# Performance work log

Measured on AMD Instinct MI355X. Metric: run time of the kernel, lower is better.

The kernel has to match this reference:

```python
import jax, jax.numpy as jnp
import numpy as np

B, L, D, HD = 4, 4096, 2048, 128

def setup_inputs() -> dict:
    key = jax.random.key(0)
    ks = jax.random.split(key, 9)
    s = 0.02  # keep logits in a sane range
    return {
        "x": jax.random.normal(ks[0], (B, L, D), jnp.float32),
        "Wq": jax.random.normal(ks[1], (D, HD), jnp.float32) * s,
        "bq": jax.random.normal(ks[2], (HD,), jnp.float32) * s,
        "Wk": jax.random.normal(ks[3], (D, HD), jnp.float32) * s,
        "bk": jax.random.normal(ks[4], (HD,), jnp.float32) * s,
        "Wv": jax.random.normal(ks[5], (D, HD), jnp.float32) * s,
        "bv": jax.random.normal(ks[6], (HD,), jnp.float32) * s,
        "Wo": jax.random.normal(ks[7], (HD, D), jnp.float32) * s,
        "bo": jax.random.normal(ks[8], (D,), jnp.float32) * s,
    }

def reference(x, Wq, bq, Wk, bk, Wv, bv, Wo, bo):
    # x: (B, L, D)
    q = x @ Wq + bq                      # (B, L, HD)
    k = x @ Wk + bk
    v = x @ Wv + bv
    hd = q.shape[-1]
    scores = jnp.einsum('bqd,bkd->bqk', q, k) / jnp.sqrt(jnp.float32(hd))
    Lq = x.shape[1]
    causal = jnp.tril(jnp.ones((Lq, Lq), dtype=bool))  # (L, L)
    scores = jnp.where(causal, scores, -jnp.inf)
    weights = jax.nn.softmax(scores, axis=-1)          # (B, L, L)
    out = jnp.einsum('bqk,bkd->bqd', weights, v)       # (B, L, HD)
    return out @ Wo + bo                               # (B, L, D)
```

## Files before the change

kernel.cpp:

```cpp
#include <hip/hip_runtime.h>

#define B_  4
#define L_  4096
#define D_  2048
#define HD_ 128
#define M_  (B_*L_)

typedef __attribute__((ext_vector_type(8))) short short8;
typedef __attribute__((ext_vector_type(4))) float f32x4;
typedef __attribute__((ext_vector_type(16))) float f32x16;
typedef __attribute__((ext_vector_type(4))) unsigned short u16x4;
typedef __attribute__((ext_vector_type(4))) unsigned int u32x4;
typedef unsigned short u16;

#define GLL16(g, l) __builtin_amdgcn_global_load_lds( \
    (const __attribute__((address_space(1))) void*)(g), \
    (__attribute__((address_space(3))) void*)(l), 16, 0, 0)

__device__ __forceinline__ u16 f2bf(float f){
  union { float f; unsigned u; } v; v.f = f;
  unsigned r = v.u + 0x7FFFu + ((v.u >> 16) & 1u);
  return (u16)(r >> 16);
}

__device__ __forceinline__ unsigned cvtpk_bf16(float a, float b){
  unsigned r;
  asm volatile("v_cvt_pk_bf16_f32 %0, %1, %2" : "=v"(r) : "v"(a), "v"(b));
  return r;
}

__global__ __launch_bounds__(256) void prep_kernel(
    const float* __restrict__ Wq, const float* __restrict__ Wk,
    const float* __restrict__ Wv, const float* __restrict__ Wo,
    u16* __restrict__ Wf_qkv, u16* __restrict__ Wf_o)
{
  __shared__ float T[64][68];
  const int tid = threadIdx.x;
  int tb = blockIdx.x;
  int mat = tb >> 6, tt = tb & 63;
  const float* src; int Rw, Cw, rt, ct;
  if (mat < 3) {
    src = (mat==0) ? Wq : (mat==1) ? Wk : Wv;
    Rw = D_; Cw = HD_; rt = tt >> 1; ct = tt & 1;
  } else {
    src = Wo;
    Rw = HD_; Cw = D_; rt = tt >> 5; ct = tt & 31;
  }
  int r0 = rt*64, c0 = ct*64;
  #pragma unroll
  for (int i=0;i<4;i++){
    int fid = i*256 + tid;
    int row = fid >> 4, c4 = (fid & 15) * 4;
    float4 v = *reinterpret_cast<const float4*>(src + (size_t)(r0+row)*Cw + c0 + c4);
    *reinterpret_cast<float4*>(&T[row][c4]) = v;
  }
  __syncthreads();
  #pragma unroll
  for (int i=0;i<2;i++){
    int sid = i*256 + tid;
    int crow = sid >> 3, k8 = (sid & 7) * 8;
    short8 o;
    #pragma unroll
    for (int j=0;j<8;j++) o[j] = (short)f2bf(T[k8+j][crow]);
    int K = r0 + k8;
    if (mat < 3) {
      int C = mat*128 + c0 + crow;
      int t2 = K >> 6, ks = (K >> 5) & 1, lh = (K >> 3) & 3;
      int g = C >> 4, l15c = C & 15;
      size_t off = ((size_t)((t2*2 + ks)*24 + g)*64 + (lh*16 + l15c))*8;
      *reinterpret_cast<short8*>(Wf_qkv + off) = o;
    } else {
      int C = c0 + crow;
      int ks = K >> 5, lh = (K >> 3) & 3;
      int g = C >> 4, l15c = C & 15;
      size_t off = ((size_t)(ks*128 + g)*64 + (lh*16 + l15c))*8;
      *reinterpret_cast<short8*>(Wf_o + off) = o;
    }
  }
}

__global__ __launch_bounds__(256, 2) void qkv_kernel(
    const float* __restrict__ x, const u16* __restrict__ Wf,
    const float* __restrict__ bq, const float* __restrict__ bk,
    const float* __restrict__ bv,
    u16* __restrict__ Q, u16* __restrict__ Kf, u16* __restrict__ Vf)
{
  const int rb = blockIdx.x;
  const int tid  = threadIdx.x;
  const int lane = tid & 63, w = tid >> 6;
  const int l15 = lane & 15, lhi = lane >> 4;
  const int row0 = rb * 32;

  __shared__ float Asm[2][32*64];

  const float* aSrc[2]; 
  #pragma unroll
  for (int i=0;i<2;i++){
    int c = w*2 + i;
    int row = c*4 + (lane >> 4);
    int k4  = (lane & 15) * 4;
    int ksrc = k4 ^ ((row & 7) << 3);
    aSrc[i] = x + (size_t)(row0 + row)*D_ + ksrc;
  }
  int offA[2][2];
  #pragma unroll
  for (int ks=0;ks<2;ks++)
    #pragma unroll
    for (int m=0;m<2;m++)
      offA[ks][m] = (m*16 + l15)*64 + ((ks*32 + lhi*8) ^ ((l15 & 7) << 3));

  const u16* wfLane = Wf + lane*8;

  f32x4 acc[2][6];
  f32x4 zero4 = {0.f,0.f,0.f,0.f};
  #pragma unroll
  for (int m=0;m<2;m++)
    #pragma unroll
    for (int n=0;n<6;n++) acc[m][n] = zero4;

  #pragma unroll
  for (int i=0;i<2;i++){
    GLL16(aSrc[i], &Asm[0][(w*2+i)*256]);
    aSrc[i] += 64;
  }
  __syncthreads();

  for (int t = 0; t < 32; ++t) {
    const int cur = t & 1;
    if (t + 1 < 32) {
      #pragma unroll
      for (int i=0;i<2;i++){
        GLL16(aSrc[i], &Asm[cur^1][(w*2+i)*256]);
        aSrc[i] += 64;
      }
    }
    const float* Ac = &Asm[cur][0];
    #pragma unroll
    for (int ks=0;ks<2;ks++){
      short8 fb[6];
      const u16* fbp = wfLane + (size_t)((t*2 + ks)*24 + w*6)*512;
      #pragma unroll
      for (int n=0;n<6;n++)
        fb[n] = *reinterpret_cast<const short8*>(fbp + n*512);
      short8 fa[2];
      #pragma unroll
      for (int m=0;m<2;m++){
        float4 f0 = *reinterpret_cast<const float4*>(Ac + offA[ks][m]);
        float4 f1 = *reinterpret_cast<const float4*>(Ac + offA[ks][m] + 4);
        union { u32x4 u; short8 s8; } tt;
        tt.u[0] = cvtpk_bf16(f0.x, f0.y);
        tt.u[1] = cvtpk_bf16(f0.z, f0.w);
        tt.u[2] = cvtpk_bf16(f1.x, f1.y);
        tt.u[3] = cvtpk_bf16(f1.z, f1.w);
        fa[m] = tt.s8;
      }
      #pragma unroll
      for (int m=0;m<2;m++)
        #pragma unroll
        for (int n=0;n<6;n++)
          acc[m][n] = __builtin_amdgcn_mfma_f32_16x16x32_bf16(fa[m], fb[n], acc[m][n], 0, 0, 0);
    }
    __syncthreads();
  }

  const float qscale = 0.08838834764831845f;
  #pragma unroll
  for (int n=0;n<6;n++){
    int col = w*96 + n*16 + l15;
    int j = col >> 7;
    int c = col & 127;
    float bi = (j==0) ? bq[c] : (j==1) ? bk[c] : bv[c];
    #pragma unroll
    for (int m=0;m<2;m++){
      int rowb = row0 + m*16 + (lhi<<2);
      int bb = rowb >> 12;
      int l0 = rowb & (L_-1);
      if (j == 0) {
        #pragma unroll
        for (int r=0;r<4;r++)
          Q[(size_t)(rowb+r)*HD_ + c] = f2bf((acc[m][n][r] + bi) * qscale);
      } else if (j == 1) {
        int ksd = c >> 4, hid = (c >> 3) & 1, jd = c & 7;
        #pragma unroll
        for (int r=0;r<4;r++){
          int l = l0 + r;
          int kt = l >> 6, k6 = l & 63;
          int n2 = k6 >> 5, l31k = k6 & 31;
          Kf[((size_t)bb*64 + kt)*8192 + (n2*8 + ksd)*512 + (hid*32 + l31k)*8 + jd]
              = f2bf(acc[m][n][r] + bi);
        }
      } else {
        int nbv = (c >> 5) & 3, l31v = c & 31;
        int kt = l0 >> 6, k6 = l0 & 63;
        int ksv = k6 >> 4, hiv = (k6 >> 3) & 1, j0 = k6 & 7;
        u16x4 v4;
        #pragma unroll
        for (int r=0;r<4;r++) v4[r] = f2bf(acc[m][n][r] + bi);
        *reinterpret_cast<u16x4*>(
            Vf + ((size_t)bb*64 + kt)*8192 + (ksv*4 + nbv)*512 + (hiv*32 + l31v)*8 + j0) = v4;
      }
    }
  }
}

__global__ __launch_bounds__(256, 2) void attn_kernel(
    const u16* __restrict__ Qg, const u16* __restrict__ Kfg,
    const u16* __restrict__ Vfg, u16* __restrict__ AOf)
{
  const int blk = blockIdx.x;
  const int xcd = blk & 7;
  const int sub = blk >> 3;
  const int b   = xcd >> 1;
  const int strip = 127 - (2*sub + (xcd & 1));
  const int q0  = strip * 32;
  const int KT  = (strip >> 1) + 1;

  const int tid = threadIdx.x, lane = tid & 63, w = tid >> 6;
  const int l31 = lane & 31;
  const int hi  = lane >> 5;

  const u16* Qb  = Qg  + (size_t)b * L_ * HD_;
  const u16* Kfb = Kfg + (size_t)b * 64 * 8192 + lane*8;
  const u16* Vfb = Vfg + (size_t)b * 64 * 8192 + lane*8;

  __shared__ __attribute__((aligned(16))) float Ol[4][32][132];
  __shared__ float Ml[4][32], Ll[4][32];

  short8 qf[8];
  #pragma unroll
  for (int ks=0; ks<8; ks++)
    qf[ks] = *reinterpret_cast<const short8*>(
        &Qb[(size_t)(q0 + l31)*HD_ + ks*16 + hi*8]);

  f32x16 O[4];
  #pragma unroll
  for (int nb=0; nb<4; nb++)
    #pragma unroll
    for (int i=0;i<16;i++) O[nb][i] = 0.f;
  float m_ = -__builtin_inff();
  float l_ = 0.f;

  for (int kt = w; kt < KT; kt += 4) {
    const u16* Kt = Kfb + (size_t)kt*8192;
    f32x16 s[2];
    #pragma unroll
    for (int n=0;n<2;n++)
      #pragma unroll
      for (int i=0;i<16;i++) s[n][i] = 0.f;
    __builtin_amdgcn_s_setprio(1);
    #pragma unroll
    for (int ks=0;ks<8;ks++)
      #pragma unroll
      for (int n=0;n<2;n++){
        short8 ka = *reinterpret_cast<const short8*>(Kt + (n*8 + ks)*512);
        s[n] = __builtin_amdgcn_mfma_f32_32x32x16_bf16(ka, qf[ks], s[n], 0, 0, 0);
      }
    __builtin_amdgcn_s_setprio(0);

    if (kt == KT-1) {
      #pragma unroll
      for (int n=0;n<2;n++)
        #pragma unroll
        for (int reg=0;reg<16;reg++){
          int key = kt*64 + n*32 + (reg&3) + 8*(reg>>2) + 4*hi;
          if (key > q0 + l31) s[n][reg] = -__builtin_inff();
        }
    }

    float pmax = s[0][0];
    #pragma unroll
    for (int n=0;n<2;n++)
      #pragma unroll
      for (int reg=0;reg<16;reg++) pmax = fmaxf(pmax, s[n][reg]);
    pmax = fmaxf(pmax, __shfl_xor(pmax, 32, 64));

    if (!__all(pmax <= m_ + 8.f)) {
      float mnew = fmaxf(m_, pmax);
      float alpha = __expf(m_ - mnew);
      m_ = mnew;
      l_ *= alpha;
      #pragma unroll
      for (int nb=0; nb<4; nb++)
        #pragma unroll
        for (int i=0;i<16;i++) O[nb][i] *= alpha;
    }

    float rsum = 0.f;
    #pragma unroll
    for (int n=0;n<2;n++)
      #pragma unroll
      for (int reg=0;reg<16;reg++){
        float p = __expf(s[n][reg] - m_);
        s[n][reg] = p;
        rsum += p;
      }
    rsum += __shfl_xor(rsum, 32, 64);
    l_ += rsum;

    unsigned c[2][8], ox[2][8];
    #pragma unroll
    for (int n=0;n<2;n++)
      #pragma unroll
      for (int i=0;i<8;i++)
        c[n][i] = cvtpk_bf16(s[n][2*i], s[n][2*i+1]);
    #pragma unroll
    for (int n=0;n<2;n++)
      #pragma unroll
      for (int i=0;i<8;i++)
        ox[n][i] = (unsigned)__shfl_xor((int)c[n][i], 32, 64);

    short8 pb[4];
    #pragma unroll
    for (int n=0;n<2;n++)
      #pragma unroll
      for (int sB=0;sB<2;sB++){
        union { u32x4 u; short8 s8; } t;
        t.u[0] = hi ? ox[n][4*sB+2] : c[n][4*sB+0];
        t.u[1] = hi ? ox[n][4*sB+3] : c[n][4*sB+1];
        t.u[2] = hi ? c[n][4*sB+2]  : ox[n][4*sB+0];
        t.u[3] = hi ? c[n][4*sB+3]  : ox[n][4*sB+1];
        pb[2*n+sB] = t.s8;
      }

    const u16* Vt2 = Vfb + (size_t)kt*8192;
    __builtin_amdgcn_s_setprio(1);
    #pragma unroll
    for (int ks=0; ks<4; ks++){
      #pragma unroll
      for (int nb=0; nb<4; nb++){
        short8 av = *reinterpret_cast<const short8*>(Vt2 + (ks*4 + nb)*512);
        O[nb] = __builtin_amdgcn_mfma_f32_32x32x16_bf16(av, pb[ks], O[nb], 0, 0, 0);
      }
    }
    __builtin_amdgcn_s_setprio(0);
  }

  if (hi == 0) { Ml[w][l31] = m_; Ll[w][l31] = l_; }
  #pragma unroll
  for (int nb=0; nb<4; nb++)
    #pragma unroll
    for (int g=0; g<4; g++){
      f32x4 v;
      v[0]=O[nb][4*g+0]; v[1]=O[nb][4*g+1]; v[2]=O[nb][4*g+2]; v[3]=O[nb][4*g+3];
      *reinterpret_cast<f32x4*>(&Ol[w][l31][nb*32 + g*8 + hi*4]) = v;
    }
  __syncthreads();

  {
    int q  = tid >> 3;
    int dc = (tid & 7) * 16;
    float mw[4], lw[4];
    float M = -__builtin_inff();
    #pragma unroll
    for (int w2=0; w2<4; w2++){ mw[w2]=Ml[w2][q]; lw[w2]=Ll[w2][q]; M = fmaxf(M, mw[w2]); }
    float den = 0.f, cw[4];
    #pragma unroll
    for (int w2=0; w2<4; w2++){ float e = __expf(mw[w2]-M); cw[w2]=e; den += lw[w2]*e; }
    float inv = 1.0f/den;
    float o[16];
    #pragma unroll
    for (int j=0;j<16;j++) o[j] = 0.f;
    #pragma unroll
    for (int w2=0; w2<4; w2++){
      #pragma unroll
      for (int g=0; g<4; g++){
        f32x4 p = *reinterpret_cast<const f32x4*>(&Ol[w2][q][dc + g*4]);
        #pragma unroll
        for (int j=0;j<4;j++) o[g*4+j] += cw[w2]*p[j];
      }
    }
    short8 st0, st1;
    #pragma unroll
    for (int j=0;j<8;j++){ st0[j] = (short)f2bf(o[j]*inv); st1[j] = (short)f2bf(o[8+j]*inv); }
    size_t rowg = (size_t)b*L_ + q0 + q;
    size_t rb2g = rowg >> 5;
    int qq = (int)(rowg & 31);
    int mA = qq >> 4, l15A = qq & 15;
    int ks0 = dc >> 5,      lh0 = (dc >> 3) & 3;
    int ks1 = (dc+8) >> 5,  lh1 = ((dc+8) >> 3) & 3;
    *reinterpret_cast<short8*>(AOf + ((rb2g*4 + ks0)*2 + mA)*512 + (lh0*16 + l15A)*8) = st0;
    *reinterpret_cast<short8*>(AOf + ((rb2g*4 + ks1)*2 + mA)*512 + (lh1*16 + l15A)*8) = st1;
  }
}

__global__ __launch_bounds__(256) void proj_kernel(
    const u16* __restrict__ AOf, const u16* __restrict__ Wf_o,
    const float* __restrict__ bo, float* __restrict__ out)
{
  const int nb  = blockIdx.x;
  const int rbk = blockIdx.y;
  const int tid = threadIdx.x, lane = tid & 63, w = tid >> 6;
  const int l15 = lane & 15, lhi = lane >> 4;

  const u16* faBase = AOf  + (size_t)rbk*8*512 + lane*8;
  const u16* fbBase = Wf_o + lane*8;

  f32x4 acc[2][4];
  f32x4 zero4 = {0.f,0.f,0.f,0.f};
  #pragma unroll
  for (int m=0;m<2;m++)
    #pragma unroll
    for (int n=0;n<4;n++) acc[m][n] = zero4;

  #pragma unroll
  for (int ks=0; ks<4; ks++){
    short8 fa[2], fb[4];
    #pragma unroll
    for (int m=0;m<2;m++)
      fa[m] = *reinterpret_cast<const short8*>(faBase + (ks*2 + m)*512);
    #pragma unroll
    for (int n=0;n<4;n++)
      fb[n] = *reinterpret_cast<const short8*>(
          fbBase + (size_t)(ks*128 + nb*16 + w*4 + n)*512);
    #pragma unroll
    for (int m=0;m<2;m++)
      #pragma unroll
      for (int n=0;n<4;n++)
        acc[m][n] = __builtin_amdgcn_mfma_f32_16x16x32_bf16(fa[m], fb[n], acc[m][n], 0, 0, 0);
  }

  #pragma unroll
  for (int n=0;n<4;n++){
    int col = nb*256 + w*64 + n*16 + l15;
    float bi = bo[col];
    #pragma unroll
    for (int m=0;m<2;m++){
      int row = rbk*32 + m*16 + (lhi<<2);
      #pragma unroll
      for (int r=0;r<4;r++)
        out[(size_t)(row+r)*D_ + col] = acc[m][n][r] + bi;
    }
  }
}

extern "C" void kernel_launch(void* const* d_in, const int* in_sizes, int n_in,
                              void* d_out, int out_size, void* d_ws, size_t ws_size,
                              hipStream_t stream) {
  const float* x  = (const float*)d_in[0];
  const float* Wq = (const float*)d_in[1];
  const float* bq = (const float*)d_in[2];
  const float* Wk = (const float*)d_in[3];
  const float* bk = (const float*)d_in[4];
  const float* Wv = (const float*)d_in[5];
  const float* bv = (const float*)d_in[6];
  const float* Wo = (const float*)d_in[7];
  const float* bo = (const float*)d_in[8];
  float* out = (float*)d_out;

  u16* ws      = (u16*)d_ws;
  u16* Wf_qkv  = ws;
  u16* Wf_o    = Wf_qkv + 3*HD_*D_;
  u16* Q       = Wf_o   + (size_t)D_*HD_;
  u16* Kf      = Q + (size_t)M_*HD_;
  u16* Vf      = Kf + (size_t)M_*HD_;
  u16* AOf     = Vf + (size_t)M_*HD_;

  prep_kernel<<<256, 256, 0, stream>>>(Wq, Wk, Wv, Wo, Wf_qkv, Wf_o);
  qkv_kernel<<<512, 256, 0, stream>>>(x, Wf_qkv, bq, bk, bv, Q, Kf, Vf);
  attn_kernel<<<512, 256, 0, stream>>>(Q, Kf, Vf, AOf);
  proj_kernel<<<dim3(8, 512), 256, 0, stream>>>(AOf, Wf_o, bo, out);
}
```

Baseline: 174.1 us.

## Enlarge QKV projection tile to 64 rows with a three-stage LDS ring

The QKV GEMM kernel now gives each block 64 rows of x instead of 32, arranged as a 2x2 wave grid where each wave computes 32 rows by 192 columns. This halves the number of times each block reads the packed weights. The two-buffer LDS pipeline becomes a three-slot ring with one barrier per iteration, and the k-step now covers 64 elements. Priority is raised around the MFMA section. Register pressure rises to 24 accumulators plus 24 B fragments per wave, and the grid shrinks to 256 blocks, which lowers occupancy and latency hiding.

```diff
diff --git a/kernel.cpp b/kernel.cpp
--- a/kernel.cpp
+++ b/kernel.cpp
@@ -88,91 +88,105 @@
   const int rb = blockIdx.x;
   const int tid  = threadIdx.x;
   const int lane = tid & 63, w = tid >> 6;
+  const int wr = w >> 1, wc = w & 1;
   const int l15 = lane & 15, lhi = lane >> 4;
-  const int row0 = rb * 32;
-
-  __shared__ float Asm[2][32*64];
-
-  const float* aSrc[2]; 
-  #pragma unroll
-  for (int i=0;i<2;i++){
-    int c = w*2 + i;
+  const int row0 = rb * 64;
+
+  __shared__ float Asm[3][64*64];
+
+  const float* gs[4];
+  #pragma unroll
+  for (int i=0;i<4;i++){
+    int c = w*4 + i;
     int row = c*4 + (lane >> 4);
-    int k4  = (lane & 15) * 4;
-    int ksrc = k4 ^ ((row & 7) << 3);
-    aSrc[i] = x + (size_t)(row0 + row)*D_ + ksrc;
-  }
-  int offA[2][2];
+    int ksrc = ((lane & 15) * 4) ^ ((row & 7) << 2);
+    gs[i] = x + (size_t)(row0 + row)*D_ + ksrc;
+  }
+  int offA[2][2][2];
   #pragma unroll
   for (int ks=0;ks<2;ks++)
     #pragma unroll
-    for (int m=0;m<2;m++)
-      offA[ks][m] = (m*16 + l15)*64 + ((ks*32 + lhi*8) ^ ((l15 & 7) << 3));
-
-  const u16* wfLane = Wf + lane*8;
-
-  f32x4 acc[2][6];
+    for (int m=0;m<2;m++){
+      int r = wr*32 + m*16 + l15;
+      int s = (r & 7) << 2;
+      int k0 = ks*32 + lhi*8;
+      offA[ks][m][0] = r*64 + (k0 ^ s);
+      offA[ks][m][1] = r*64 + ((k0 + 4) ^ s);
+    }
+
+  #pragma unroll
+  for (int i=0;i<4;i++) GLL16(gs[i],      &Asm[0][(w*4+i)*256]);
+  #pragma unroll
+  for (int i=0;i<4;i++) GLL16(gs[i] + 64, &Asm[1][(w*4+i)*256]);
+  #pragma unroll
+  for (int i=0;i<4;i++) gs[i] += 128;
+  asm volatile("s_waitcnt vmcnt(4)" ::: "memory");
+
+  const u16* bptr = Wf + (size_t)(wc*12)*512 + lane*8;
+
+  f32x4 acc[2][12];
   f32x4 zero4 = {0.f,0.f,0.f,0.f};
   #pragma unroll
   for (int m=0;m<2;m++)
     #pragma unroll
-    for (int n=0;n<6;n++) acc[m][n] = zero4;
-
-  #pragma unroll
-  for (int i=0;i<2;i++){
-    GLL16(aSrc[i], &Asm[0][(w*2+i)*256]);
-    aSrc[i] += 64;
-  }
-  __syncthreads();
-
+    for (int n=0;n<12;n++) acc[m][n] = zero4;
+
+  int rs = 0, ws2 = 2;
   for (int t = 0; t < 32; ++t) {
-    const int cur = t & 1;
-    if (t + 1 < 32) {
-      #pragma unroll
-      for (int i=0;i<2;i++){
-        GLL16(aSrc[i], &Asm[cur^1][(w*2+i)*256]);
-        aSrc[i] += 64;
-      }
-    }
-    const float* Ac = &Asm[cur][0];
-    #pragma unroll
-    for (int ks=0;ks<2;ks++){
-      short8 fb[6];
-      const u16* fbp = wfLane + (size_t)((t*2 + ks)*24 + w*6)*512;
-      #pragma unroll
-      for (int n=0;n<6;n++)
-        fb[n] = *reinterpret_cast<const short8*>(fbp + n*512);
-      short8 fa[2];
+    __builtin_amdgcn_s_barrier();
+    short8 fb0[12], fb1[12];
+    #pragma unroll
+    for (int n=0;n<12;n++) fb0[n] = *reinterpret_cast<const short8*>(bptr + (size_t)n*512);
+    #pragma unroll
+    for (int n=0;n<12;n++) fb1[n] = *reinterpret_cast<const short8*>(bptr + (size_t)(24+n)*512);
+    bptr += (size_t)48*512;
+    __builtin_amdgcn_sched_barrier(0);
+    if (t < 30) {
+      #pragma unroll
+      for (int i=0;i<4;i++){ GLL16(gs[i], &Asm[ws2][(w*4+i)*256]); gs[i] += 64; }
+    }
+    __builtin_amdgcn_sched_barrier(0);
+    const float* Ac = &Asm[rs][0];
+    short8 fa[2][2];
+    #pragma unroll
+    for (int ks=0;ks<2;ks++)
       #pragma unroll
       for (int m=0;m<2;m++){
-        float4 f0 = *reinterpret_cast<const float4*>(Ac + offA[ks][m]);
-        float4 f1 = *reinterpret_cast<const float4*>(Ac + offA[ks][m] + 4);
+        float4 f0 = *reinterpret_cast<const float4*>(Ac + offA[ks][m][0]);
+        float4 f1 = *reinterpret_cast<const float4*>(Ac + offA[ks][m][1]);
         union { u32x4 u; short8 s8; } tt;
         tt.u[0] = cvtpk_bf16(f0.x, f0.y);
         tt.u[1] = cvtpk_bf16(f0.z, f0.w);
         tt.u[2] = cvtpk_bf16(f1.x, f1.y);
         tt.u[3] = cvtpk_bf16(f1.z, f1.w);
-        fa[m] = tt.s8;
-      }
-      #pragma unroll
-      for (int m=0;m<2;m++)
-        #pragma unroll
-        for (int n=0;n<6;n++)
-          acc[m][n] = __builtin_amdgcn_mfma_f32_16x16x32_bf16(fa[m], fb[n], acc[m][n], 0, 0, 0);
-    }
-    __syncthreads();
+        fa[ks][m] = tt.s8;
+      }
+    __builtin_amdgcn_s_setprio(1);
+    #pragma unroll
+    for (int m=0;m<2;m++)
+      #pragma unroll
+      for (int n=0;n<12;n++)
+        acc[m][n] = __builtin_amdgcn_mfma_f32_16x16x32_bf16(fa[0][m], fb0[n], acc[m][n], 0, 0, 0);
+    #pragma unroll
+    for (int m=0;m<2;m++)
+      #pragma unroll
+      for (int n=0;n<12;n++)
+        acc[m][n] = __builtin_amdgcn_mfma_f32_16x16x32_bf16(fa[1][m], fb1[n], acc[m][n], 0, 0, 0);
+    __builtin_amdgcn_s_setprio(0);
+    rs  = (rs  == 2) ? 0 : rs  + 1;
+    ws2 = (ws2 == 2) ? 0 : ws2 + 1;
   }
 
   const float qscale = 0.08838834764831845f;
   #pragma unroll
-  for (int n=0;n<6;n++){
-    int col = w*96 + n*16 + l15;
+  for (int n=0;n<12;n++){
+    int col = wc*192 + n*16 + l15;
     int j = col >> 7;
     int c = col & 127;
     float bi = (j==0) ? bq[c] : (j==1) ? bk[c] : bv[c];
     #pragma unroll
     for (int m=0;m<2;m++){
-      int rowb = row0 + m*16 + (lhi<<2);
+      int rowb = row0 + wr*32 + m*16 + (lhi<<2);
       int bb = rowb >> 12;
       int l0 = rowb & (L_-1);
       if (j == 0) {
@@ -456,7 +470,7 @@
   u16* AOf     = Vf + (size_t)M_*HD_;
 
   prep_kernel<<<256, 256, 0, stream>>>(Wq, Wk, Wv, Wo, Wf_qkv, Wf_o);
-  qkv_kernel<<<512, 256, 0, stream>>>(x, Wf_qkv, bq, bk, bv, Q, Kf, Vf);
+  qkv_kernel<<<256, 256, 0, stream>>>(x, Wf_qkv, bq, bk, bv, Q, Kf, Vf);
   attn_kernel<<<512, 256, 0, stream>>>(Q, Kf, Vf, AOf);
   proj_kernel<<<dim3(8, 512), 256, 0, stream>>>(AOf, Wf_o, bo, out);
 }
```

Result: slower. 178.5 us (+2.5%).

## Stage QKV weights in LDS and convert x to bf16 during register prefetch

Applied to the files above, without the earlier changes.

Restructures the QKV projection main loop. x is now prefetched into registers two steps ahead, converted to bf16 and stored into a bf16 LDS tile in MFMA fragment layout. The packed weight fragments are staged into double-buffered LDS with global_load_lds instead of being read directly from global memory on every step. The loop runs 64 steps of K=32 instead of 32 steps of K=64 and raises wave priority around the MFMA block. This is meant to hide weight and x load latency behind the matrix math, at the cost of much more LDS per block (about 52KB), which may limit occupancy, and one barrier per 32-wide K step.

```diff
diff --git a/kernel.cpp b/kernel.cpp
--- a/kernel.cpp
+++ b/kernel.cpp
@@ -10,6 +10,7 @@
 typedef __attribute__((ext_vector_type(4))) float f32x4;
 typedef __attribute__((ext_vector_type(16))) float f32x16;
 typedef __attribute__((ext_vector_type(4))) unsigned short u16x4;
+typedef __attribute__((ext_vector_type(2))) unsigned int u32x2;
 typedef __attribute__((ext_vector_type(4))) unsigned int u32x4;
 typedef unsigned short u16;
 
@@ -91,25 +92,17 @@
   const int l15 = lane & 15, lhi = lane >> 4;
   const int row0 = rb * 32;
 
-  __shared__ float Asm[2][32*64];
-
-  const float* aSrc[2]; 
-  #pragma unroll
-  for (int i=0;i<2;i++){
-    int c = w*2 + i;
-    int row = c*4 + (lane >> 4);
-    int k4  = (lane & 15) * 4;
-    int ksrc = k4 ^ ((row & 7) << 3);
-    aSrc[i] = x + (size_t)(row0 + row)*D_ + ksrc;
-  }
-  int offA[2][2];
-  #pragma unroll
-  for (int ks=0;ks<2;ks++)
-    #pragma unroll
-    for (int m=0;m<2;m++)
-      offA[ks][m] = (m*16 + l15)*64 + ((ks*32 + lhi*8) ^ ((l15 & 7) << 3));
-
-  const u16* wfLane = Wf + lane*8;
+  __shared__ u16 Asm[2][1024];
+  __shared__ u16 Bsm[2][24*512];
+
+  const int aR = tid >> 3, acc8 = tid & 7;
+  const int ah = acc8 >> 1, ahalf = acc8 & 1;
+  const int aWrOff = (aR >> 4)*512 + (ah*16 + (aR & 15))*8 + ahalf*4;
+  const float* xsrc = x + (size_t)(row0 + aR)*D_ + acc8*4;
+
+  const u16* bSrcBase = Wf + (size_t)(w*6)*512 + lane*8;
+  u16* bDst0 = &Bsm[0][(w*6)*512];
+  u16* bDst1 = &Bsm[1][(w*6)*512];
 
   f32x4 acc[2][6];
   f32x4 zero4 = {0.f,0.f,0.f,0.f};
@@ -118,49 +111,51 @@
     #pragma unroll
     for (int n=0;n<6;n++) acc[m][n] = zero4;
 
-  #pragma unroll
-  for (int i=0;i<2;i++){
-    GLL16(aSrc[i], &Asm[0][(w*2+i)*256]);
-    aSrc[i] += 64;
-  }
+  float4 xa = *reinterpret_cast<const float4*>(xsrc);
+  #pragma unroll
+  for (int i=0;i<6;i++)
+    GLL16(bSrcBase + (size_t)i*512, bDst0 + i*512);
+  {
+    u16x4 a4;
+    a4[0] = f2bf(xa.x); a4[1] = f2bf(xa.y); a4[2] = f2bf(xa.z); a4[3] = f2bf(xa.w);
+    *reinterpret_cast<u16x4*>(&Asm[0][aWrOff]) = a4;
+  }
+  xa = *reinterpret_cast<const float4*>(xsrc + 32);
   __syncthreads();
 
-  for (int t = 0; t < 32; ++t) {
-    const int cur = t & 1;
-    if (t + 1 < 32) {
-      #pragma unroll
-      for (int i=0;i<2;i++){
-        GLL16(aSrc[i], &Asm[cur^1][(w*2+i)*256]);
-        aSrc[i] += 64;
-      }
-    }
-    const float* Ac = &Asm[cur][0];
-    #pragma unroll
-    for (int ks=0;ks<2;ks++){
-      short8 fb[6];
-      const u16* fbp = wfLane + (size_t)((t*2 + ks)*24 + w*6)*512;
+  for (int t = 0; t < 64; ++t) {
+    const int cur = t & 1, nxt = cur ^ 1;
+    float4 xb;
+    if (t + 2 < 64)
+      xb = *reinterpret_cast<const float4*>(xsrc + (t+2)*32);
+    if (t + 1 < 64) {
+      const u16* bs = bSrcBase + (size_t)(t+1)*24*512;
+      u16* bd = (nxt ? bDst1 : bDst0);
+      #pragma unroll
+      for (int i=0;i<6;i++)
+        GLL16(bs + (size_t)i*512, bd + i*512);
+    }
+    short8 fa[2], fb[6];
+    #pragma unroll
+    for (int m=0;m<2;m++)
+      fa[m] = *reinterpret_cast<const short8*>(&Asm[cur][m*512 + lane*8]);
+    #pragma unroll
+    for (int n=0;n<6;n++)
+      fb[n] = *reinterpret_cast<const short8*>(&Bsm[cur][(w*6+n)*512 + lane*8]);
+    __builtin_amdgcn_s_setprio(1);
+    #pragma unroll
+    for (int m=0;m<2;m++)
       #pragma unroll
       for (int n=0;n<6;n++)
-        fb[n] = *reinterpret_cast<const short8*>(fbp + n*512);
-      short8 fa[2];
-      #pragma unroll
-      for (int m=0;m<2;m++){
-        float4 f0 = *reinterpret_cast<const float4*>(Ac + offA[ks][m]);
-        float4 f1 = *reinterpret_cast<const float4*>(Ac + offA[ks][m] + 4);
-        union { u32x4 u; short8 s8; } tt;
-        tt.u[0] = cvtpk_bf16(f0.x, f0.y);
-        tt.u[1] = cvtpk_bf16(f0.z, f0.w);
-        tt.u[2] = cvtpk_bf16(f1.x, f1.y);
-        tt.u[3] = cvtpk_bf16(f1.z, f1.w);
-        fa[m] = tt.s8;
-      }
-      #pragma unroll
-      for (int m=0;m<2;m++)
-        #pragma unroll
-        for (int n=0;n<6;n++)
-          acc[m][n] = __builtin_amdgcn_mfma_f32_16x16x32_bf16(fa[m], fb[n], acc[m][n], 0, 0, 0);
+        acc[m][n] = __builtin_amdgcn_mfma_f32_16x16x32_bf16(fa[m], fb[n], acc[m][n], 0, 0, 0);
+    __builtin_amdgcn_s_setprio(0);
+    if (t + 1 < 64) {
+      u16x4 a4;
+      a4[0] = f2bf(xa.x); a4[1] = f2bf(xa.y); a4[2] = f2bf(xa.z); a4[3] = f2bf(xa.w);
+      *reinterpret_cast<u16x4*>(&Asm[nxt][aWrOff]) = a4;
     }
     __syncthreads();
+    xa = xb;
   }
 
   const float qscale = 0.08838834764831845f;
```

New measurement: 180.7 us. 1.04x slower.
